# Kernel tuning notes

Hardware: AMD Instinct MI355X
Metric: run time of the kernel (lower is better)

The kernel has to match this reference:

```python
import jax, jax.numpy as jnp
import numpy as np

B, S_SRC, S_TRG = 128, 512, 128
VIN, VOUT = 128, 128
E, H = 128, 256          # embed, encoder hidden
HD = 2 * H               # decoder hidden = 512 (concat of bi-dir encoder states)
DENC = 2 * H             # encoder output feature dim = 512


def setup_inputs() -> dict:
    key = jax.random.key(0)
    ks = jax.random.split(key, 20)
    g = lambda k, shape: (jax.random.normal(k, shape, jnp.float32) * 0.05)
    inp = {
        "src": jax.random.randint(ks[0], (B, S_SRC), 0, VIN, jnp.int32),
        "trg": jax.random.randint(ks[1], (B, S_TRG), 0, VOUT, jnp.int32),
        # encoder
        "enc_emb": g(ks[2], (VIN, E)),
        "enc_Wih_f": g(ks[3], (4 * H, E)),
        "enc_Whh_f": g(ks[4], (4 * H, H)),
        "enc_b_f": g(ks[5], (4 * H,)),
        "enc_Wih_b": g(ks[6], (4 * H, E)),
        "enc_Whh_b": g(ks[7], (4 * H, H)),
        "enc_b_b": g(ks[8], (4 * H,)),
        # decoder
        "dec_emb": g(ks[9], (VOUT, E)),
        "dec_Wih": g(ks[10], (4 * HD, E + DENC)),
        "dec_Whh": g(ks[11], (4 * HD, HD)),
        "dec_b": g(ks[12], (4 * HD,)),
        # attention: Linear(dec_hid + enc_dim -> HD), v: Linear(HD -> 1)
        "attn_W": g(ks[13], (HD + DENC, HD)),
        "attn_b": g(ks[14], (HD,)),
        "attn_v": g(ks[15], (HD,)),
        # output projection
        "out_W": g(ks[16], (HD, VOUT)),
        "out_b": g(ks[17], (VOUT,)),
    }
    return inp


def _lstm_cell(h, c, x, Wih, Whh, b):
    gates = x @ Wih.T + h @ Whh.T + b               # [B, 4H]
    i, f, gg, o = jnp.split(gates, 4, axis=-1)       # PyTorch gate order i,f,g,o
    i, f, o = jax.nn.sigmoid(i), jax.nn.sigmoid(f), jax.nn.sigmoid(o)
    c = f * c + i * jnp.tanh(gg)
    h = o * jnp.tanh(c)
    return h, c


def _lstm_scan(xs, Wih, Whh, b, reverse=False):
    # xs: [S, B, E] -> hs: [S, B, H] (time-aligned), plus final (h, c)
    Bn, Hn = xs.shape[1], Whh.shape[1]
    init = (jnp.zeros((Bn, Hn), xs.dtype), jnp.zeros((Bn, Hn), xs.dtype))
    def step(carry, x):
        h, c = _lstm_cell(carry[0], carry[1], x, Wih, Whh, b)
        return (h, c), h
    (h, c), hs = jax.lax.scan(step, init, xs, reverse=reverse)
    return hs, h, c


def reference(src, trg, enc_emb, enc_Wih_f, enc_Whh_f, enc_b_f,
              enc_Wih_b, enc_Whh_b, enc_b_b, dec_emb, dec_Wih, dec_Whh,
              dec_b, attn_W, attn_b, attn_v, out_W, out_b):
    # ----- encoder (bidirectional LSTM) -----
    emb = enc_emb[src]                                # [B, S, E]
    xs = jnp.swapaxes(emb, 0, 1)                      # [S, B, E]
    hs_f, hf, cf = _lstm_scan(xs, enc_Wih_f, enc_Whh_f, enc_b_f, reverse=False)
    hs_b, hb, cb = _lstm_scan(xs, enc_Wih_b, enc_Whh_b, enc_b_b, reverse=True)
    enc_out = jnp.swapaxes(jnp.concatenate([hs_f, hs_b], -1), 0, 1)  # [B, S, 2H]
    hidden = jnp.concatenate([hf, hb], -1)            # [B, HD]  (hidden.view(1,B,-1))
    cell = jnp.concatenate([cf, cb], -1)              # [B, HD]

    # attention linear split: energy = tanh([h, enc] @ W + b)
    Wh, We = attn_W[:HD], attn_W[HD:]
    enc_proj = jnp.einsum("bsd,de->bse", enc_out, We)  # [B, S, HD] precomputed

    def dec_step(carry, tok):
        h, c = carry
        e = jnp.tanh(h[:, None, :] @ Wh + enc_proj + attn_b)     # [B, S, HD]
        scores = jnp.einsum("bse,e->bs", e, attn_v)              # [B, S]
        aw = jax.nn.softmax(scores, axis=1)
        ctx = jnp.einsum("bs,bsd->bd", aw, enc_out)              # [B, DENC]
        x = jnp.concatenate([dec_emb[tok], ctx], -1)             # [B, E+DENC]
        h, c = _lstm_cell(h, c, x, dec_Wih, dec_Whh, dec_b)
        logits = h @ out_W + out_b                               # [B, VOUT]
        return (h, c), logits

    # teacher forcing (ratio=1.0): input at step t is trg[:, t-1], t = 1..T-1
    toks = jnp.swapaxes(trg[:, :-1], 0, 1)            # [T-1, B]
    _, logits = jax.lax.scan(dec_step, (hidden, cell), toks)
    logits = jnp.swapaxes(logits, 0, 1)               # [B, T-1, VOUT]
    outputs = jnp.concatenate(
        [jnp.zeros((src.shape[0], 1, VOUT), logits.dtype), logits], axis=1)
    return outputs
```

## Files before the change

kernel.cpp:

```cpp
#include <hip/hip_runtime.h>


typedef _Float16 f16;
typedef _Float16 half8 __attribute__((ext_vector_type(8)));
typedef float f32x4 __attribute__((ext_vector_type(4)));
typedef char char8v __attribute__((ext_vector_type(8)));

#define MFMA16(a, b, c) __builtin_amdgcn_mfma_f32_16x16x32_f16((a), (b), (c), 0, 0, 0)

#define PSCALE (2.5f / 127.f)
#define PINV   (127.f / 2.5f)

__device__ __forceinline__ float fsig(float x) {
    return __builtin_amdgcn_rcpf(1.f + __expf(-x));
}
__device__ __forceinline__ float ftanh(float x) {
    return 1.f - 2.f * __builtin_amdgcn_rcpf(1.f + __expf(2.f * x));
}
__device__ __forceinline__ int frag_idx(int m, int k, int KS) {
    return (((m >> 4) * KS + (k >> 5)) * 64 + (((k >> 3) & 3) * 16 + (m & 15))) * 8 + (k & 7);
}

__global__ void k_zero(unsigned* __restrict__ s)
{
    for (int z = threadIdx.x; z < 4112; z += 256) s[z] = 0u;
}

__global__ __launch_bounds__(256) void k_prep(
    const float* __restrict__ attn_W, const float* __restrict__ out_W,
    const float* __restrict__ enc_emb,
    const float* __restrict__ wihf, const float* __restrict__ wihb,
    const float* __restrict__ whhf, const float* __restrict__ whhb,
    const float* __restrict__ dec_emb, const float* __restrict__ dec_wih,
    const float* __restrict__ dec_whh,
    f16* __restrict__ WhT_sw, f16* __restrict__ outWT_sw,
    f16* __restrict__ whhf_sw, f16* __restrict__ whhb_sw,
    f16* __restrict__ decwih_sw, f16* __restrict__ decwhh_sw,
    f16* __restrict__ WeT, f16* __restrict__ emb16,
    f16* __restrict__ wihf16, f16* __restrict__ wihb16,
    f16* __restrict__ decemb16, float* __restrict__ out)
{
    long i = (long)blockIdx.x * 256 + threadIdx.x;
    if (i >= 3784704L) return;
    long idx = i;
    if (idx < 262144) {
        int j = idx & 7, lane = (idx >> 3) & 63, c = lane & 15, q = lane >> 4;
        int ks = (idx >> 9) & 15, nt = idx >> 13;
        WhT_sw[idx] = (f16)attn_W[(ks * 32 + q * 8 + j) * 512 + nt * 16 + c];
        return;
    }
    idx -= 262144;
    if (idx < 65536) {
        int j = idx & 7, lane = (idx >> 3) & 63, c = lane & 15, q = lane >> 4;
        int ks = (idx >> 9) & 15, nt = idx >> 13;
        outWT_sw[idx] = (f16)out_W[(ks * 32 + q * 8 + j) * 128 + nt * 16 + c];
        return;
    }
    idx -= 65536;
    if (idx < 262144) {
        int j = idx & 7, lane = (idx >> 3) & 63, c = lane & 15, q = lane >> 4;
        int ks = (idx >> 9) & 7, nt = idx >> 12;
        whhf_sw[idx] = (f16)whhf[(nt * 16 + c) * 256 + ks * 32 + q * 8 + j];
        return;
    }
    idx -= 262144;
    if (idx < 262144) {
        int j = idx & 7, lane = (idx >> 3) & 63, c = lane & 15, q = lane >> 4;
        int ks = (idx >> 9) & 7, nt = idx >> 12;
        whhb_sw[idx] = (f16)whhb[(nt * 16 + c) * 256 + ks * 32 + q * 8 + j];
        return;
    }
    idx -= 262144;
    if (idx < 1310720) {
        int j = idx & 7, lane = (idx >> 3) & 63, c = lane & 15, q = lane >> 4;
        int r2 = idx >> 9; int ks = r2 % 20, nt = r2 / 20;
        decwih_sw[idx] = (f16)dec_wih[(nt * 16 + c) * 640 + ks * 32 + q * 8 + j];
        return;
    }
    idx -= 1310720;
    if (idx < 1048576) {
        int j = idx & 7, lane = (idx >> 3) & 63, c = lane & 15, q = lane >> 4;
        int ks = (idx >> 9) & 15, nt = idx >> 13;
        decwhh_sw[idx] = (f16)dec_whh[(nt * 16 + c) * 512 + ks * 32 + q * 8 + j];
        return;
    }
    idx -= 1048576;
    if (idx < 262144) { int e = idx >> 9, d = idx & 511; WeT[idx] = (f16)attn_W[(512 + d) * 512 + e]; return; }
    idx -= 262144;
    if (idx < 16384)  { emb16[idx] = (f16)enc_emb[idx]; return; }
    idx -= 16384;
    if (idx < 131072) { wihf16[idx] = (f16)wihf[idx]; return; }
    idx -= 131072;
    if (idx < 131072) { wihb16[idx] = (f16)wihb[idx]; return; }
    idx -= 131072;
    if (idx < 16384)  { decemb16[idx] = (f16)dec_emb[idx]; return; }
    idx -= 16384;
    if (idx < 16384)  { int b = idx >> 7, v = idx & 127; out[b * 16384 + v] = 0.f; return; }
}

__global__ __launch_bounds__(256) void k_vocab(
    const f16* __restrict__ emb, const f16* __restrict__ wihf,
    const f16* __restrict__ wihb, const float* __restrict__ bf_,
    const float* __restrict__ bb_, f16* __restrict__ xg_vocab)
{
    int bn = blockIdx.x;
    int tid = threadIdx.x, wave = tid >> 6, lane = tid & 63;
    int col = lane & 15, quad = lane >> 4;
    int wr = wave >> 1, wc = wave & 1;

    f32x4 acc[4][4] = {};
    for (int ks = 0; ks < 4; ++ks) {
        int k0 = ks * 32 + quad * 8;
        half8 a[4], bfr[4];
        for (int i = 0; i < 4; ++i)
            a[i] = *(const half8*)(emb + (wr * 64 + i * 16 + col) * 128 + k0);
        for (int j = 0; j < 4; ++j) {
            int n = bn * 128 + wc * 64 + j * 16 + col;
            const f16* wp = (n < 1024) ? (wihf + n * 128) : (wihb + (n - 1024) * 128);
            bfr[j] = *(const half8*)(wp + k0);
        }
        for (int i = 0; i < 4; ++i)
            for (int j = 0; j < 4; ++j)
                acc[i][j] = MFMA16(a[i], bfr[j], acc[i][j]);
    }
    for (int j = 0; j < 4; ++j) {
        int n = bn * 128 + wc * 64 + j * 16 + col;
        float bias = (n < 1024) ? bf_[n] : bb_[n - 1024];
        for (int i = 0; i < 4; ++i) {
            int vbase = wr * 64 + i * 16 + quad * 4;
            for (int r = 0; r < 4; ++r)
                xg_vocab[(vbase + r) * 2048 + n] = (f16)(acc[i][j][r] + bias);
        }
    }
}

__global__ __launch_bounds__(512, 1) void k_enc(
    const int* __restrict__ src, const f16* __restrict__ xg_vocab,
    const f16* __restrict__ whhf_sw, const f16* __restrict__ whhb_sw,
    f16* __restrict__ enc_out, f16* __restrict__ hdec0, float* __restrict__ c_ws)
{
    int blk = blockIdx.x;
    int dir = blk >> 3, bbase = (blk & 7) * 16;
    int tid = threadIdx.x, wave = tid >> 6, lane = tid & 63;
    int col = lane & 15, quad = lane >> 4;
    const f16* whh = dir ? whhb_sw : whhf_sw;

    __shared__ f16 hb[16][264];
    __shared__ f16 xvb[16][1032];
    __shared__ int stall[8192];

    for (int z = tid; z < 16 * 264; z += 512) ((f16*)hb)[z] = (f16)0.f;
    for (int z = tid; z < 8192; z += 512) stall[z] = src[bbase * 512 + z];
    float cc[2][4] = {};

    half8 bst[32];
    #pragma unroll
    for (int g = 0; g < 2; ++g)
        #pragma unroll
        for (int nt = 0; nt < 2; ++nt)
            #pragma unroll
            for (int kk = 0; kk < 8; ++kk) {
                int tile = g * 16 + wave * 2 + nt;
                bst[(g * 2 + nt) * 8 + kk] =
                    *(const half8*)(whh + ((tile * 8 + kk) * 64 + lane) * 8);
            }
    __syncthreads();

    int xrow = tid >> 7, xoff = (tid & 127) * 8;
    half8 xr[4];
    {
        int ts0 = dir ? 511 : 0;
        #pragma unroll
        for (int it = 0; it < 4; ++it) {
            int row = it * 4 + xrow;
            int tok = stall[row * 512 + ts0];
            xr[it] = *(const half8*)(xg_vocab + tok * 2048 + dir * 1024 + xoff);
        }
    }

    int ts_prev = 0;
    for (int t = 0; t < 512; ++t) {
        int ts = dir ? (511 - t) : t;

        if (t > 0) {
            int b = tid >> 5, seg = tid & 31;
            *(half8*)(enc_out + ((size_t)(bbase + b) * 512 + ts_prev) * 512 + dir * 256 + seg * 8) =
                *(const half8*)(&hb[b][seg * 8]);
        }
        #pragma unroll
        for (int it = 0; it < 4; ++it)
            *(half8*)(&xvb[it * 4 + xrow][xoff]) = xr[it];
        half8 a[8];
        #pragma unroll
        for (int kk = 0; kk < 8; ++kk)
            a[kk] = *(const half8*)(&hb[col][kk * 32 + quad * 8]);
        __syncthreads();

        if (t < 511) {
            int tsn = dir ? (510 - t) : (t + 1);
            #pragma unroll
            for (int it = 0; it < 4; ++it) {
                int row = it * 4 + xrow;
                int tok = stall[row * 512 + tsn];
                xr[it] = *(const half8*)(xg_vocab + tok * 2048 + dir * 1024 + xoff);
            }
        }

        f32x4 acc[4][2] = {};
        #pragma unroll
        for (int kk = 0; kk < 8; ++kk) {
            half8 bv[4];
            #pragma unroll
            for (int g = 2; g < 4; ++g)
                #pragma unroll
                for (int nt = 0; nt < 2; ++nt) {
                    int tile = g * 16 + wave * 2 + nt;
                    bv[(g - 2) * 2 + nt] =
                        *(const half8*)(whh + ((tile * 8 + kk) * 64 + lane) * 8);
                }
            #pragma unroll
            for (int g = 0; g < 2; ++g)
                #pragma unroll
                for (int nt = 0; nt < 2; ++nt)
                    acc[g][nt] = MFMA16(a[kk], bst[(g * 2 + nt) * 8 + kk], acc[g][nt]);
            #pragma unroll
            for (int g = 2; g < 4; ++g)
                #pragma unroll
                for (int nt = 0; nt < 2; ++nt)
                    acc[g][nt] = MFMA16(a[kk], bv[(g - 2) * 2 + nt], acc[g][nt]);
        }

        #pragma unroll
        for (int nt = 0; nt < 2; ++nt) {
            int hcol = wave * 32 + nt * 16 + col;
            #pragma unroll
            for (int r = 0; r < 4; ++r) {
                int b = quad * 4 + r;
                float gi = (float)xvb[b][0 * 256 + hcol] + acc[0][nt][r];
                float gf = (float)xvb[b][1 * 256 + hcol] + acc[1][nt][r];
                float gg = (float)xvb[b][2 * 256 + hcol] + acc[2][nt][r];
                float go = (float)xvb[b][3 * 256 + hcol] + acc[3][nt][r];
                float ig = fsig(gi), fg = fsig(gf), g2 = ftanh(gg), og = fsig(go);
                float cv = fg * cc[nt][r] + ig * g2;
                cc[nt][r] = cv;
                float h = og * ftanh(cv);
                hb[b][hcol] = (f16)h;
            }
        }
        __syncthreads();
        ts_prev = ts;
    }

    {
        int b = tid >> 5, seg = tid & 31;
        *(half8*)(enc_out + ((size_t)(bbase + b) * 512 + ts_prev) * 512 + dir * 256 + seg * 8) =
            *(const half8*)(&hb[b][seg * 8]);
    }
    #pragma unroll
    for (int nt = 0; nt < 2; ++nt) {
        int hcol = wave * 32 + nt * 16 + col;
        #pragma unroll
        for (int r = 0; r < 4; ++r) {
            int b = quad * 4 + r;
            int m = bbase + b, k = dir * 256 + hcol;
            hdec0[frag_idx(m, k, 16)] = hb[b][hcol];
            c_ws[m * 512 + k] = cc[nt][r];
        }
    }
}

__global__ __launch_bounds__(256) void k_proj(
    const f16* __restrict__ enc_out, const f16* __restrict__ WeT,
    char* __restrict__ proj8)
{
    int blk = blockIdx.x;
    int bm = blk & 511, bn = blk >> 9;
    int tid = threadIdx.x, wave = tid >> 6, lane = tid & 63;
    int col = lane & 15, quad = lane >> 4;
    int wr = wave >> 1, wc = wave & 1;

    f32x4 acc[4][4] = {};
    for (int ks = 0; ks < 16; ++ks) {
        int k0 = ks * 32 + quad * 8;
        half8 a[4], bfr[4];
        for (int i = 0; i < 4; ++i) {
            int m = bm * 128 + wr * 64 + i * 16 + col;
            a[i] = *(const half8*)(enc_out + (size_t)m * 512 + k0);
        }
        for (int j = 0; j < 4; ++j) {
            int n = bn * 128 + wc * 64 + j * 16 + col;
            bfr[j] = *(const half8*)(WeT + n * 512 + k0);
        }
        for (int i = 0; i < 4; ++i)
            for (int j = 0; j < 4; ++j)
                acc[i][j] = MFMA16(a[i], bfr[j], acc[i][j]);
    }
    for (int j = 0; j < 4; ++j) {
        int n = bn * 128 + wc * 64 + j * 16 + col;
        for (int i = 0; i < 4; ++i) {
            int mbase = bm * 128 + wr * 64 + i * 16 + quad * 4;
            for (int r = 0; r < 4; ++r) {
                float v = acc[i][j][r] * PINV;
                int q = (int)rintf(v);
                q = (q > 127) ? 127 : ((q < -127) ? -127 : q);
                proj8[(size_t)(mbase + r) * 512 + n] = (char)q;
            }
        }
    }
}

__global__ __launch_bounds__(256) void k_qinit(
    const f16* __restrict__ h0_sw, const f16* __restrict__ WhT_sw,
    float* __restrict__ qpart)
{
    int j = blockIdx.x;
    int tid = threadIdx.x, wave = tid >> 6, lane = tid & 63;
    int col = lane & 15, quad = lane >> 4;
    half8 a[2];
    #pragma unroll
    for (int i = 0; i < 2; ++i)
        a[i] = *(const half8*)(h0_sw + (((wave * 2 + i) * 16 + j) * 64 + lane) * 8);
    for (int nt = 0; nt < 32; ++nt) {
        half8 bfr = *(const half8*)(WhT_sw + ((nt * 16 + j) * 64 + lane) * 8);
        f32x4 q0 = {}, q1 = {};
        q0 = MFMA16(a[0], bfr, q0);
        q1 = MFMA16(a[1], bfr, q1);
        #pragma unroll
        for (int r = 0; r < 4; ++r) {
            qpart[(j * 128 + wave * 32 + quad * 4 + r) * 512 + nt * 16 + col] = q0[r];
            qpart[(j * 128 + wave * 32 + 16 + quad * 4 + r) * 512 + nt * 16 + col] = q1[r];
        }
    }
}

__global__ __launch_bounds__(512, 4) void k_step(
    const char* __restrict__ proj8, const f16* __restrict__ enc_out,
    float* __restrict__ qpart, const float* __restrict__ attn_bp,
    const float* __restrict__ attn_vp, const int* __restrict__ trg,
    const f16* __restrict__ dec_emb, f16* __restrict__ x_sw,
    float* __restrict__ part_m, float* __restrict__ part_l,
    float* __restrict__ part_ctx, f16* __restrict__ hdec0,
    f16* __restrict__ hdec1, const f16* __restrict__ wih_sw,
    const f16* __restrict__ whh_sw, const float* __restrict__ dec_bp,
    float* __restrict__ c_ws, f16* __restrict__ hhist_sw,
    const f16* __restrict__ WhT_sw, unsigned* __restrict__ flags, int tt)
{
    int blk = blockIdx.x;
    int tid = threadIdx.x, wave = tid >> 6, lane = tid & 63;
    int col = lane & 15, quad = lane >> 4;

    __shared__ float q[512];
    __shared__ float sc[256];
    __shared__ float ctxred[8][512];
    __shared__ float wred[8], wred2[8];
    __shared__ f16 hsl[64][40];
    __shared__ float gm[64][2];
    __shared__ int islast;

    if (blk < 32) {
        int tg = tt - 1;
        if (tg >= 0) {
            int j = blk >> 1, mh = blk & 1;
            if (tid < 64) {
                int bb = mh * 64 + tid;
                float m0 = part_m[bb * 2 + 0], m1 = part_m[bb * 2 + 1];
                float l0 = part_l[bb * 2 + 0], l1 = part_l[bb * 2 + 1];
                float M = fmaxf(m0, m1);
                float g0 = __expf(m0 - M), g1 = __expf(m1 - M);
                float inv = 1.f / (g0 * l0 + g1 * l1);
                gm[tid][0] = g0 * inv;
                gm[tid][1] = g1 * inv;
            }
            __syncthreads();
            for (int z = tid; z < 32768; z += 512) {
                int lr = z >> 9, d = z & 511;
                int bb = mh * 64 + lr;
                float c = gm[lr][0] * part_ctx[(size_t)(bb * 2 + 0) * 512 + d]
                        + gm[lr][1] * part_ctx[(size_t)(bb * 2 + 1) * 512 + d];
                x_sw[frag_idx(bb, 128 + d, 20)] = (f16)c;
            }
            __syncthreads();

            if (tid < 256) {
                const f16* hprev = (tg & 1) ? hdec1 : hdec0;
                f16* hnext = (tg & 1) ? hdec0 : hdec1;

                f32x4 acc[8] = {};
                for (int ks = 0; ks < 36; ++ks) {
                    int mtile = mh * 4 + wave;
                    half8 a = (ks < 20)
                        ? *(const half8*)(x_sw + ((mtile * 20 + ks) * 64 + lane) * 8)
                        : *(const half8*)(hprev + ((mtile * 16 + (ks - 20)) * 64 + lane) * 8);
                    half8 bv[8];
                    #pragma unroll
                    for (int jt = 0; jt < 8; ++jt) {
                        int g = jt >> 1, u2 = jt & 1;
                        int ntile = g * 32 + j * 2 + u2;
                        bv[jt] = (ks < 20)
                            ? *(const half8*)(wih_sw + ((ntile * 20 + ks) * 64 + lane) * 8)
                            : *(const half8*)(whh_sw + ((ntile * 16 + (ks - 20)) * 64 + lane) * 8);
                    }
                    #pragma unroll
                    for (int jt = 0; jt < 8; ++jt)
                        acc[jt] = MFMA16(a, bv[jt], acc[jt]);
                }
                float bias[8];
                #pragma unroll
                for (int jt = 0; jt < 8; ++jt) {
                    int g = jt >> 1, u2 = jt & 1;
                    bias[jt] = dec_bp[g * 512 + j * 32 + u2 * 16 + col];
                }
                #pragma unroll
                for (int r = 0; r < 4; ++r) {
                    int lb = wave * 16 + quad * 4 + r;
                    int bb = mh * 64 + lb;
                    #pragma unroll
                    for (int u2 = 0; u2 < 2; ++u2) {
                        int hl = u2 * 16 + col, hcol = j * 32 + hl;
                        float gi = acc[0 + u2][r] + bias[0 + u2];
                        float gf = acc[2 + u2][r] + bias[2 + u2];
                        float gg = acc[4 + u2][r] + bias[4 + u2];
                        float go = acc[6 + u2][r] + bias[6 + u2];
                        float ig = fsig(gi), fg = fsig(gf), g2 = ftanh(gg), og = fsig(go);
                        float cv = fg * c_ws[bb * 512 + hcol] + ig * g2;
                        c_ws[bb * 512 + hcol] = cv;
                        float h = og * ftanh(cv);
                        f16 h16 = (f16)h;
                        int fidx = frag_idx(bb, hcol, 16);
                        hnext[fidx] = h16;
                        hhist_sw[tg * 65536 + fidx] = h16;
                        hsl[lb][hl] = h16;
                    }
                }
                half8 aq = *(const half8*)(&hsl[wave * 16 + col][quad * 8]);
                for (int nt = 0; nt < 32; ++nt) {
                    half8 bq = *(const half8*)(WhT_sw + ((nt * 16 + j) * 64 + lane) * 8);
                    f32x4 q0 = {};
                    q0 = MFMA16(aq, bq, q0);
                    #pragma unroll
                    for (int r = 0; r < 4; ++r)
                        qpart[(j * 128 + mh * 64 + wave * 16 + quad * 4 + r) * 512 + nt * 16 + col] = q0[r];
                }
            }

            __syncthreads();
            if (tid == 0) {
                unsigned old = __hip_atomic_fetch_add(flags, 1u, __ATOMIC_ACQ_REL,
                                                      __HIP_MEMORY_SCOPE_AGENT);
                islast = (old == (unsigned)(32 * tt - 1)) ? 1 : 0;
            }
            __syncthreads();
            if (islast && tid < 256)
                __hip_atomic_store(flags + 16 + tid * 16, (unsigned)tt,
                                   __ATOMIC_RELEASE, __HIP_MEMORY_SCOPE_AGENT);
        }
        return;
    }

    int ab = blk - 32;
    int b = ab >> 1, sh = ab & 1;
    int sbase = sh * 256;

    float vreg[8];
    #pragma unroll
    for (int u = 0; u < 8; ++u) vreg[u] = attn_vp[lane * 8 + u];
    float abias = attn_bp[tid];

    if (tt > 0) {
        if (tid == 0) {
            while (__hip_atomic_load(flags + 16 + ab * 16, __ATOMIC_RELAXED,
                                     __HIP_MEMORY_SCOPE_AGENT) < (unsigned)tt)
                __builtin_amdgcn_s_sleep(16);
            (void)__hip_atomic_load(flags + 16 + ab * 16, __ATOMIC_ACQUIRE,
                                    __HIP_MEMORY_SCOPE_AGENT);
        }
        __syncthreads();
    }

    {
        float s = abias;
        #pragma unroll
        for (int jj = 0; jj < 16; ++jj) s += qpart[(jj * 128 + b) * 512 + tid];
        q[tid] = s;
    }
    __syncthreads();

    float qreg[8];
    #pragma unroll
    for (int u = 0; u < 8; ++u) qreg[u] = q[lane * 8 + u];

    for (int ib = 0; ib < 4; ++ib) {
        char8v p[8];
        #pragma unroll
        for (int z = 0; z < 8; ++z) {
            int sl = (ib * 8 + z) * 8 + wave;
            p[z] = *(const char8v*)(proj8 + ((size_t)b * 512 + sbase + sl) * 512 + lane * 8);
        }
        #pragma unroll
        for (int z = 0; z < 8; ++z) {
            int sl = (ib * 8 + z) * 8 + wave;
            float part = 0.f;
            #pragma unroll
            for (int u = 0; u < 8; ++u)
                part += vreg[u] * ftanh(fmaf((float)p[z][u], PSCALE, qreg[u]));
            #pragma unroll
            for (int o = 32; o; o >>= 1) part += __shfl_xor(part, o);
            if (lane == 0) sc[sl] = part;
        }
    }
    __syncthreads();

    float s0 = (tid < 256) ? sc[tid] : -__builtin_inff();
    float mv = s0;
    #pragma unroll
    for (int o = 32; o; o >>= 1) mv = fmaxf(mv, __shfl_xor(mv, o));
    if (lane == 0) wred[wave] = mv;
    __syncthreads();
    float M = wred[0];
    #pragma unroll
    for (int w = 1; w < 8; ++w) M = fmaxf(M, wred[w]);
    float e0 = (tid < 256) ? __expf(s0 - M) : 0.f;
    if (tid < 256) sc[tid] = e0;
    float sm = e0;
    #pragma unroll
    for (int o = 32; o; o >>= 1) sm += __shfl_xor(sm, o);
    if (lane == 0) wred2[wave] = sm;
    __syncthreads();
    float lsum = wred2[0];
    #pragma unroll
    for (int w = 1; w < 8; ++w) lsum += wred2[w];

    float a8[8] = {};
    for (int ib = 0; ib < 4; ++ib) {
        half8 ev[8];
        float wgt[8];
        #pragma unroll
        for (int z = 0; z < 8; ++z) {
            int sl = (ib * 8 + z) * 8 + wave;
            ev[z] = *(const half8*)(enc_out + ((size_t)b * 512 + sbase + sl) * 512 + lane * 8);
            wgt[z] = sc[sl];
        }
        #pragma unroll
        for (int z = 0; z < 8; ++z)
            #pragma unroll
            for (int u = 0; u < 8; ++u) a8[u] += wgt[z] * (float)ev[z][u];
    }
    #pragma unroll
    for (int u = 0; u < 8; ++u) ctxred[wave][lane * 8 + u] = a8[u];
    __syncthreads();
    float cp = 0.f;
    #pragma unroll
    for (int w = 0; w < 8; ++w) cp += ctxred[w][tid];
    part_ctx[(size_t)ab * 512 + tid] = cp;
    if (tid == 0) { part_m[ab] = M; part_l[ab] = lsum; }

    if (sh == 0 && tid < 128) {
        int tok = trg[b * 128 + tt];
        x_sw[frag_idx(b, tid, 20)] = dec_emb[tok * 128 + tid];
    }
}

__global__ __launch_bounds__(256) void k_gates(
    f16* __restrict__ x_sw, const f16* __restrict__ hprev_sw,
    const f16* __restrict__ wih_sw, const f16* __restrict__ whh_sw,
    const float* __restrict__ dec_b, float* __restrict__ c_ws,
    f16* __restrict__ hnext_sw, f16* __restrict__ hhist_sw,
    const f16* __restrict__ WhT_sw, float* __restrict__ qpart,
    const float* __restrict__ part_m, const float* __restrict__ part_l,
    const float* __restrict__ part_ctx, int t)
{
    int jb = blockIdx.x;
    int j = jb >> 1, mh = jb & 1;
    int tid = threadIdx.x, wave = tid >> 6, lane = tid & 63;
    int col = lane & 15, quad = lane >> 4;
    __shared__ f16 hsl[64][40];
    __shared__ float gm[64][2];

    if (tid < 64) {
        int bb = mh * 64 + tid;
        float m0 = part_m[bb * 2 + 0], m1 = part_m[bb * 2 + 1];
        float l0 = part_l[bb * 2 + 0], l1 = part_l[bb * 2 + 1];
        float M = fmaxf(m0, m1);
        float g0 = __expf(m0 - M), g1 = __expf(m1 - M);
        float inv = 1.f / (g0 * l0 + g1 * l1);
        gm[tid][0] = g0 * inv;
        gm[tid][1] = g1 * inv;
    }
    __syncthreads();
    for (int z = tid; z < 32768; z += 256) {
        int lr = z >> 9, d = z & 511;
        int bb = mh * 64 + lr;
        float c = gm[lr][0] * part_ctx[(size_t)(bb * 2 + 0) * 512 + d]
                + gm[lr][1] * part_ctx[(size_t)(bb * 2 + 1) * 512 + d];
        x_sw[frag_idx(bb, 128 + d, 20)] = (f16)c;
    }
    __syncthreads();

    f32x4 acc[8] = {};
    for (int ks = 0; ks < 36; ++ks) {
        int mtile = mh * 4 + wave;
        half8 a = (ks < 20)
            ? *(const half8*)(x_sw + ((mtile * 20 + ks) * 64 + lane) * 8)
            : *(const half8*)(hprev_sw + ((mtile * 16 + (ks - 20)) * 64 + lane) * 8);
        half8 bv[8];
        #pragma unroll
        for (int jt = 0; jt < 8; ++jt) {
            int g = jt >> 1, u2 = jt & 1;
            int ntile = g * 32 + j * 2 + u2;
            bv[jt] = (ks < 20)
                ? *(const half8*)(wih_sw + ((ntile * 20 + ks) * 64 + lane) * 8)
                : *(const half8*)(whh_sw + ((ntile * 16 + (ks - 20)) * 64 + lane) * 8);
        }
        #pragma unroll
        for (int jt = 0; jt < 8; ++jt)
            acc[jt] = MFMA16(a, bv[jt], acc[jt]);
    }
    float bias[8];
    #pragma unroll
    for (int jt = 0; jt < 8; ++jt) {
        int g = jt >> 1, u2 = jt & 1;
        bias[jt] = dec_b[g * 512 + j * 32 + u2 * 16 + col];
    }
    #pragma unroll
    for (int r = 0; r < 4; ++r) {
        int lb = wave * 16 + quad * 4 + r;
        int bb = mh * 64 + lb;
        #pragma unroll
        for (int u2 = 0; u2 < 2; ++u2) {
            int hl = u2 * 16 + col, hcol = j * 32 + hl;
            float gi = acc[0 + u2][r] + bias[0 + u2];
            float gf = acc[2 + u2][r] + bias[2 + u2];
            float gg = acc[4 + u2][r] + bias[4 + u2];
            float go = acc[6 + u2][r] + bias[6 + u2];
            float ig = fsig(gi), fg = fsig(gf), g2 = ftanh(gg), og = fsig(go);
            float cv = fg * c_ws[bb * 512 + hcol] + ig * g2;
            c_ws[bb * 512 + hcol] = cv;
            float h = og * ftanh(cv);
            f16 h16 = (f16)h;
            int fidx = frag_idx(bb, hcol, 16);
            hnext_sw[fidx] = h16;
            hhist_sw[t * 65536 + fidx] = h16;
            hsl[lb][hl] = h16;
        }
    }
    half8 aq = *(const half8*)(&hsl[wave * 16 + col][quad * 8]);
    for (int nt = 0; nt < 32; ++nt) {
        half8 bq = *(const half8*)(WhT_sw + ((nt * 16 + j) * 64 + lane) * 8);
        f32x4 q0 = {};
        q0 = MFMA16(aq, bq, q0);
        #pragma unroll
        for (int r = 0; r < 4; ++r)
            qpart[(j * 128 + mh * 64 + wave * 16 + quad * 4 + r) * 512 + nt * 16 + col] = q0[r];
    }
}

__global__ __launch_bounds__(256) void k_logits(
    const f16* __restrict__ hhist_sw, const f16* __restrict__ outWT_sw,
    const float* __restrict__ out_b, float* __restrict__ out)
{
    int bt = blockIdx.x;
    int tid = threadIdx.x, wave = tid >> 6, lane = tid & 63;
    int col = lane & 15, quad = lane >> 4;
    f32x4 acc[2][8] = {};
    for (int ks = 0; ks < 16; ++ks) {
        half8 a[2];
        #pragma unroll
        for (int i = 0; i < 2; ++i)
            a[i] = *(const half8*)(hhist_sw + bt * 65536 + (((wave * 2 + i) * 16 + ks) * 64 + lane) * 8);
        half8 bv[8];
        #pragma unroll
        for (int jt = 0; jt < 8; ++jt)
            bv[jt] = *(const half8*)(outWT_sw + ((jt * 16 + ks) * 64 + lane) * 8);
        #pragma unroll
        for (int jt = 0; jt < 8; ++jt) {
            acc[0][jt] = MFMA16(a[0], bv[jt], acc[0][jt]);
            acc[1][jt] = MFMA16(a[1], bv[jt], acc[1][jt]);
        }
    }
    #pragma unroll
    for (int jt = 0; jt < 8; ++jt) {
        float bias = out_b[jt * 16 + col];
        #pragma unroll
        for (int i = 0; i < 2; ++i)
            #pragma unroll
            for (int r = 0; r < 4; ++r) {
                int br = wave * 32 + i * 16 + quad * 4 + r;
                out[br * 16384 + (bt + 1) * 128 + jt * 16 + col] = acc[i][jt][r] + bias;
            }
    }
}

extern "C" void kernel_launch(void* const* d_in, const int* in_sizes, int n_in,
                              void* d_out, int out_size, void* d_ws, size_t ws_size,
                              hipStream_t stream)
{
    (void)in_sizes; (void)n_in; (void)out_size;
    if (ws_size < 130000000) return;

    const int*   src     = (const int*)d_in[0];
    const int*   trg     = (const int*)d_in[1];
    const float* enc_emb = (const float*)d_in[2];
    const float* wihf    = (const float*)d_in[3];
    const float* whhf    = (const float*)d_in[4];
    const float* bf_     = (const float*)d_in[5];
    const float* wihb    = (const float*)d_in[6];
    const float* whhb    = (const float*)d_in[7];
    const float* bb_     = (const float*)d_in[8];
    const float* dec_emb = (const float*)d_in[9];
    const float* dec_wih = (const float*)d_in[10];
    const float* dec_whh = (const float*)d_in[11];
    const float* dec_b   = (const float*)d_in[12];
    const float* attn_W  = (const float*)d_in[13];
    const float* attn_b  = (const float*)d_in[14];
    const float* attn_v  = (const float*)d_in[15];
    const float* out_W   = (const float*)d_in[16];
    const float* out_b   = (const float*)d_in[17];
    float* out = (float*)d_out;

    char* p = (char*)d_ws;
    auto carve = [&](size_t n) { char* r = p; p += ((n + 255) & ~(size_t)255); return r; };
    f16*   enc_out   = (f16*)  carve(67108864);
    char*  proj8     = (char*) carve(33554432);
    f16*   WhT_sw    = (f16*)  carve(524288);
    f16*   WeT       = (f16*)  carve(524288);
    f16*   outWT_sw  = (f16*)  carve(131072);
    f16*   emb16     = (f16*)  carve(32768);
    f16*   wihf16    = (f16*)  carve(262144);
    f16*   wihb16    = (f16*)  carve(262144);
    f16*   whhf_sw   = (f16*)  carve(524288);
    f16*   whhb_sw   = (f16*)  carve(524288);
    f16*   decemb16  = (f16*)  carve(32768);
    f16*   decwih_sw = (f16*)  carve(2621440);
    f16*   decwhh_sw = (f16*)  carve(2097152);
    float* qpart     = (float*)carve(4194304);
    f16*   hdec0     = (f16*)  carve(131072);
    f16*   hdec1     = (f16*)  carve(131072);
    float* c_ws      = (float*)carve(262144);
    f16*   x_sw      = (f16*)  carve(163840);
    f16*   hhist_sw  = (f16*)  carve(16646144);
    f16*   xg_vocab  = (f16*)  carve(524288);
    float* part_m    = (float*)carve(2048);
    float* part_l    = (float*)carve(2048);
    float* part_ctx  = (float*)carve(524288);
    unsigned* flagsv = (unsigned*)carve(16448);

    k_zero<<<1, 256, 0, stream>>>(flagsv);
    k_prep<<<14784, 256, 0, stream>>>(attn_W, out_W, enc_emb, wihf, wihb, whhf, whhb,
                                      dec_emb, dec_wih, dec_whh,
                                      WhT_sw, outWT_sw, whhf_sw, whhb_sw,
                                      decwih_sw, decwhh_sw, WeT, emb16,
                                      wihf16, wihb16, decemb16, out);
    k_vocab<<<16, 256, 0, stream>>>(emb16, wihf16, wihb16, bf_, bb_, xg_vocab);
    k_enc<<<16, 512, 0, stream>>>(src, xg_vocab, whhf_sw, whhb_sw, enc_out, hdec0, c_ws);
    k_proj<<<2048, 256, 0, stream>>>(enc_out, WeT, proj8);
    k_qinit<<<16, 256, 0, stream>>>(hdec0, WhT_sw, qpart);

    for (int tt = 0; tt < 127; ++tt)
        k_step<<<288, 512, 0, stream>>>(proj8, enc_out, qpart, attn_b, attn_v,
                                        trg, decemb16, x_sw, part_m, part_l,
                                        part_ctx, hdec0, hdec1, decwih_sw,
                                        decwhh_sw, dec_b, c_ws, hhist_sw,
                                        WhT_sw, flagsv, tt);
    k_gates<<<32, 256, 0, stream>>>(x_sw, hdec0, decwih_sw, decwhh_sw, dec_b,
                                    c_ws, hdec1, hhist_sw, WhT_sw, qpart,
                                    part_m, part_l, part_ctx, 126);

    k_logits<<<127, 256, 0, stream>>>(hhist_sw, outWT_sw, out_b, out);
}
```

Baseline: 12.81 ms.

## Double-buffer encoder LSTM LDS state to use one barrier per step

The encoder recurrence now ping-pongs the hidden-state and input-gate LDS buffers, so each timestep needs a single barrier instead of two. The barrier is a custom LDS-only wait that does not drain outstanding global stores. To fit the doubled LDS the token table is narrowed to 16-bit, and fewer Whh fragments stay resident in registers (one gate group instead of two) while more are streamed from global/L2 each step. This trades extra per-step weight loads for less synchronisation and lower register pressure.

```diff
diff --git a/kernel.cpp b/kernel.cpp
--- a/kernel.cpp
+++ b/kernel.cpp
@@ -19,6 +19,13 @@
 }
 __device__ __forceinline__ int frag_idx(int m, int k, int KS) {
     return (((m >> 4) * KS + (k >> 5)) * 64 + (((k >> 3) & 3) * 16 + (m & 15))) * 8 + (k & 7);
+}
+
+__device__ __forceinline__ void lds_barrier() {
+    asm volatile("s_waitcnt lgkmcnt(0)" ::: "memory");
+    __builtin_amdgcn_sched_barrier(0);
+    __builtin_amdgcn_s_barrier();
+    __builtin_amdgcn_sched_barrier(0);
 }
 
 __global__ void k_zero(unsigned* __restrict__ s)
@@ -145,25 +152,22 @@
     int col = lane & 15, quad = lane >> 4;
     const f16* whh = dir ? whhb_sw : whhf_sw;
 
-    __shared__ f16 hb[16][264];
-    __shared__ f16 xvb[16][1032];
-    __shared__ int stall[8192];
-
-    for (int z = tid; z < 16 * 264; z += 512) ((f16*)hb)[z] = (f16)0.f;
-    for (int z = tid; z < 8192; z += 512) stall[z] = src[bbase * 512 + z];
+    __shared__ f16 hb[2][16][264];
+    __shared__ f16 xvb[2][16][1032];
+    __shared__ unsigned short stall[8192];
+
+    for (int z = tid; z < 2 * 16 * 264; z += 512) ((f16*)hb)[z] = (f16)0.f;
+    for (int z = tid; z < 8192; z += 512) stall[z] = (unsigned short)src[bbase * 512 + z];
     float cc[2][4] = {};
 
-    half8 bst[32];
-    #pragma unroll
-    for (int g = 0; g < 2; ++g)
-        #pragma unroll
-        for (int nt = 0; nt < 2; ++nt)
-            #pragma unroll
-            for (int kk = 0; kk < 8; ++kk) {
-                int tile = g * 16 + wave * 2 + nt;
-                bst[(g * 2 + nt) * 8 + kk] =
-                    *(const half8*)(whh + ((tile * 8 + kk) * 64 + lane) * 8);
-            }
+    half8 bst[16];
+    #pragma unroll
+    for (int nt = 0; nt < 2; ++nt)
+        #pragma unroll
+        for (int kk = 0; kk < 8; ++kk) {
+            int tile = wave * 2 + nt;
+            bst[nt * 8 + kk] = *(const half8*)(whh + ((tile * 8 + kk) * 64 + lane) * 8);
+        }
     __syncthreads();
 
     int xrow = tid >> 7, xoff = (tid & 127) * 8;
@@ -176,25 +180,16 @@
             int tok = stall[row * 512 + ts0];
             xr[it] = *(const half8*)(xg_vocab + tok * 2048 + dir * 1024 + xoff);
         }
-    }
+        #pragma unroll
+        for (int it = 0; it < 4; ++it)
+            *(half8*)(&xvb[0][it * 4 + xrow][xoff]) = xr[it];
+    }
+    __syncthreads();
 
     int ts_prev = 0;
     for (int t = 0; t < 512; ++t) {
         int ts = dir ? (511 - t) : t;
-
-        if (t > 0) {
-            int b = tid >> 5, seg = tid & 31;
-            *(half8*)(enc_out + ((size_t)(bbase + b) * 512 + ts_prev) * 512 + dir * 256 + seg * 8) =
-                *(const half8*)(&hb[b][seg * 8]);
-        }
-        #pragma unroll
-        for (int it = 0; it < 4; ++it)
-            *(half8*)(&xvb[it * 4 + xrow][xoff]) = xr[it];
-        half8 a[8];
-        #pragma unroll
-        for (int kk = 0; kk < 8; ++kk)
-            a[kk] = *(const half8*)(&hb[col][kk * 32 + quad * 8]);
-        __syncthreads();
+        int cur = t & 1, prv = cur ^ 1;
 
         if (t < 511) {
             int tsn = dir ? (510 - t) : (t + 1);
@@ -206,28 +201,37 @@
             }
         }
 
+        if (t > 0) {
+            int b = tid >> 5, seg = tid & 31;
+            *(half8*)(enc_out + ((size_t)(bbase + b) * 512 + ts_prev) * 512 + dir * 256 + seg * 8) =
+                *(const half8*)(&hb[prv][b][seg * 8]);
+        }
+
+        half8 a[8];
+        #pragma unroll
+        for (int kk = 0; kk < 8; ++kk)
+            a[kk] = *(const half8*)(&hb[prv][col][kk * 32 + quad * 8]);
+
         f32x4 acc[4][2] = {};
         #pragma unroll
         for (int kk = 0; kk < 8; ++kk) {
-            half8 bv[4];
-            #pragma unroll
-            for (int g = 2; g < 4; ++g)
+            half8 bv[6];
+            #pragma unroll
+            for (int g = 1; g < 4; ++g)
                 #pragma unroll
                 for (int nt = 0; nt < 2; ++nt) {
                     int tile = g * 16 + wave * 2 + nt;
-                    bv[(g - 2) * 2 + nt] =
+                    bv[(g - 1) * 2 + nt] =
                         *(const half8*)(whh + ((tile * 8 + kk) * 64 + lane) * 8);
                 }
             #pragma unroll
-            for (int g = 0; g < 2; ++g)
+            for (int nt = 0; nt < 2; ++nt)
+                acc[0][nt] = MFMA16(a[kk], bst[nt * 8 + kk], acc[0][nt]);
+            #pragma unroll
+            for (int g = 1; g < 4; ++g)
                 #pragma unroll
                 for (int nt = 0; nt < 2; ++nt)
-                    acc[g][nt] = MFMA16(a[kk], bst[(g * 2 + nt) * 8 + kk], acc[g][nt]);
-            #pragma unroll
-            for (int g = 2; g < 4; ++g)
-                #pragma unroll
-                for (int nt = 0; nt < 2; ++nt)
-                    acc[g][nt] = MFMA16(a[kk], bv[(g - 2) * 2 + nt], acc[g][nt]);
+                    acc[g][nt] = MFMA16(a[kk], bv[(g - 1) * 2 + nt], acc[g][nt]);
         }
 
         #pragma unroll
@@ -236,25 +240,32 @@
             #pragma unroll
             for (int r = 0; r < 4; ++r) {
                 int b = quad * 4 + r;
-                float gi = (float)xvb[b][0 * 256 + hcol] + acc[0][nt][r];
-                float gf = (float)xvb[b][1 * 256 + hcol] + acc[1][nt][r];
-                float gg = (float)xvb[b][2 * 256 + hcol] + acc[2][nt][r];
-                float go = (float)xvb[b][3 * 256 + hcol] + acc[3][nt][r];
+                float gi = (float)xvb[cur][b][0 * 256 + hcol] + acc[0][nt][r];
+                float gf = (float)xvb[cur][b][1 * 256 + hcol] + acc[1][nt][r];
+                float gg = (float)xvb[cur][b][2 * 256 + hcol] + acc[2][nt][r];
+                float go = (float)xvb[cur][b][3 * 256 + hcol] + acc[3][nt][r];
                 float ig = fsig(gi), fg = fsig(gf), g2 = ftanh(gg), og = fsig(go);
                 float cv = fg * cc[nt][r] + ig * g2;
                 cc[nt][r] = cv;
                 float h = og * ftanh(cv);
-                hb[b][hcol] = (f16)h;
+                hb[cur][b][hcol] = (f16)h;
             }
         }
-        __syncthreads();
+
+        if (t < 511) {
+            #pragma unroll
+            for (int it = 0; it < 4; ++it)
+                *(half8*)(&xvb[prv][it * 4 + xrow][xoff]) = xr[it];
+        }
+
+        lds_barrier();
         ts_prev = ts;
     }
 
     {
         int b = tid >> 5, seg = tid & 31;
         *(half8*)(enc_out + ((size_t)(bbase + b) * 512 + ts_prev) * 512 + dir * 256 + seg * 8) =
-            *(const half8*)(&hb[b][seg * 8]);
+            *(const half8*)(&hb[1][b][seg * 8]);
     }
     #pragma unroll
     for (int nt = 0; nt < 2; ++nt) {
@@ -263,7 +274,7 @@
         for (int r = 0; r < 4; ++r) {
             int b = quad * 4 + r;
             int m = bbase + b, k = dir * 256 + hcol;
-            hdec0[frag_idx(m, k, 16)] = hb[b][hcol];
+            hdec0[frag_idx(m, k, 16)] = hb[1][b][hcol];
             c_ws[m * 512 + k] = cc[nt][r];
         }
     }
```

Result: faster. 12.46 ms (-2.7%).
